# Performance work log

Measured on AMD Instinct MI355X. Metric: run time of the kernel, lower is better.

Reference implementation:

```python
import jax, jax.numpy as jnp
import numpy as np

LN_EPS = 1e-5


def setup_inputs() -> dict:
    key = jax.random.key(0)
    ks = jax.random.split(key, 6)
    N, E, D = 100000, 600000, 128
    x = jax.random.normal(ks[0], (N, D), dtype=jnp.float32)
    edge_index = jax.random.randint(ks[1], (2, E), 0, N, dtype=jnp.int64)
    dropout_mask = jax.random.uniform(ks[2], (N, D), dtype=jnp.float32)
    ln_gamma = jnp.ones((D,), dtype=jnp.float32)
    ln_beta = jnp.zeros((D,), dtype=jnp.float32)
    W_l = jax.random.normal(ks[3], (D, D), dtype=jnp.float32) / np.sqrt(D)
    b_l = jnp.zeros((D,), dtype=jnp.float32)
    W_r = jax.random.normal(ks[4], (D, D), dtype=jnp.float32) / np.sqrt(D)
    return {"x": x, "edge_index": edge_index, "dropout_mask": dropout_mask,
            "ln_gamma": ln_gamma, "ln_beta": ln_beta,
            "W_l": W_l, "b_l": b_l, "W_r": W_r}


def reference(x, edge_index, dropout_mask, ln_gamma, ln_beta, W_l, b_l, W_r):
    N = x.shape[0]
    # LayerNorm (elementwise affine) -> ReLU -> dropout mask
    mu = jnp.mean(x, axis=-1, keepdims=True)
    var = jnp.mean(jnp.square(x - mu), axis=-1, keepdims=True)
    h = (x - mu) * jax.lax.rsqrt(var + LN_EPS) * ln_gamma + ln_beta
    h = jax.nn.relu(h) * dropout_mask  # [N, D]
    # SAGEConv with mean aggregation: messages flow src -> dst
    src, dst = edge_index[0], edge_index[1]
    agg = jax.ops.segment_sum(h[src], dst, num_segments=N)  # [N, D]
    cnt = jax.ops.segment_sum(jnp.ones_like(dst, dtype=h.dtype), dst,
                              num_segments=N)
    mean_agg = agg / jnp.maximum(cnt, 1.0)[:, None]
    # out = lin_l(mean_agg) + lin_r(h); PyG stores weights as [out, in]
    return mean_agg @ W_l.T + b_l + h @ W_r.T
```

## Files before the change

### kernel.cpp

```cpp
#include <hip/hip_runtime.h>

#define LN_EPS 1e-5f
#define D 128
#define SCAN_CHUNK 1024
#define LDSA_STRIDE 264

typedef __attribute__((ext_vector_type(4))) float f32x4;
typedef __attribute__((ext_vector_type(8))) short bf16x8;

static __device__ __forceinline__ ushort f2bf(float f) {
    union { float f; unsigned u; } a; a.f = f;
    unsigned r = a.u + 0x7FFF + ((a.u >> 16) & 1);
    return (ushort)(r >> 16);
}
static __device__ __forceinline__ float bf2f(ushort u) {
    union { unsigned u; float f; } a; a.u = ((unsigned)u) << 16;
    return a.f;
}

__global__ void prep_w(const float* __restrict__ Wl,
                       const float* __restrict__ Wr,
                       ushort* __restrict__ Bfrag,
                       int* __restrict__ hist,
                       int* __restrict__ csums, int N) {
    int t = blockIdx.x * blockDim.x + threadIdx.x;
    if (t < 8 * 8 * 64 * 8) {
        int i    = t & 7;
        int lane = (t >> 3) & 63;
        int jb   = (t >> 9) & 7;
        int ks   = t >> 12;
        int k = ks * 32 + (lane >> 4) * 8 + i;
        int j = jb * 16 + (lane & 15);
        float v = (k < D) ? Wl[j * D + k] : Wr[j * D + (k - D)];
        Bfrag[t] = f2bf(v);
    }
    if (t < 128) csums[t] = 0;
    for (int i = t; i < N; i += gridDim.x * blockDim.x) hist[i] = 0;
}

__global__ void hist_k(const int* __restrict__ ei, int* __restrict__ hist, int E) {
    int base = (blockIdx.x * blockDim.x + threadIdx.x) * 4;
    const int* dst = ei + E;
    if (base + 3 < E) {
        int4 d = *(const int4*)(dst + base);
        atomicAdd(&hist[d.x], 1);
        atomicAdd(&hist[d.y], 1);
        atomicAdd(&hist[d.z], 1);
        atomicAdd(&hist[d.w], 1);
    } else {
        for (int i = base; i < E && i < base + 4; i++)
            atomicAdd(&hist[dst[i]], 1);
    }
}

__global__ void scan_all(const int* __restrict__ hist, int* __restrict__ offs,
                         int* __restrict__ cursor, int* __restrict__ csums, int N) {
    __shared__ int lds[256];
    __shared__ int base_s;
    int base = blockIdx.x * SCAN_CHUNK;
    int t = threadIdx.x;
    int idx0 = base + t * 4;
    int v[4];
#pragma unroll
    for (int i = 0; i < 4; i++) {
        int idx = idx0 + i;
        v[i] = (idx < N) ? hist[idx] : 0;
    }
    lds[t] = v[0] + v[1] + v[2] + v[3];
    __syncthreads();
    for (int off = 1; off < 256; off <<= 1) {
        int add = (t >= off) ? lds[t - off] : 0;
        __syncthreads();
        lds[t] += add;
        __syncthreads();
    }
    int run = (t == 0) ? 0 : lds[t - 1];
    if (t == 255)
        __hip_atomic_store(&csums[blockIdx.x], lds[255] | 0x40000000,
                           __ATOMIC_RELEASE, __HIP_MEMORY_SCOPE_AGENT);
    if (t < 64) {
        int acc = 0;
        for (int c = t; c < (int)blockIdx.x; c += 64) {
            int w;
            do {
                w = __hip_atomic_load(&csums[c], __ATOMIC_ACQUIRE,
                                      __HIP_MEMORY_SCOPE_AGENT);
            } while (!(w & 0x40000000));
            acc += w & 0x3FFFFFFF;
        }
#pragma unroll
        for (int off = 32; off > 0; off >>= 1) acc += __shfl_xor(acc, off);
        if (t == 0) base_s = acc;
    }
    __syncthreads();
    run += base_s;
#pragma unroll
    for (int i = 0; i < 4; i++) {
        int idx = idx0 + i;
        if (idx < N) {
            offs[idx] = run;
            cursor[idx] = run;
        }
        run += v[i];
    }
}

__global__ void sort_edges(const int* __restrict__ ei, int* __restrict__ cursor,
                           int* __restrict__ sorted_src, int E) {
    int base = (blockIdx.x * blockDim.x + threadIdx.x) * 4;
    if (base >= E) return;
    if (base + 3 < E) {
        int4 d = *(const int4*)(ei + E + base);
        int4 s = *(const int4*)(ei + base);
        int p0 = atomicAdd(&cursor[d.x], 1);
        int p1 = atomicAdd(&cursor[d.y], 1);
        int p2 = atomicAdd(&cursor[d.z], 1);
        int p3 = atomicAdd(&cursor[d.w], 1);
        sorted_src[p0] = s.x;
        sorted_src[p1] = s.y;
        sorted_src[p2] = s.z;
        sorted_src[p3] = s.w;
    } else {
        for (int e = base; e < E; e++) {
            int pos = atomicAdd(&cursor[ei[E + e]], 1);
            sorted_src[pos] = ei[e];
        }
    }
}

__global__ void ln_k(const float* __restrict__ x,
                     const float* __restrict__ mask,
                     const float* __restrict__ gamma,
                     const float* __restrict__ beta,
                     ushort* __restrict__ hbf, int N) {
    int tid  = threadIdx.x;
    int lane = tid & 63;
    int wid  = ((int)blockIdx.x * 256 + tid) >> 6;
    int g2   = lane >> 4;
    int sl   = lane & 15;
    int node = wid * 4 + g2;
    if (node >= N) return;

    const float* xr = x + (size_t)node * D + sl * 8;
    f32x4 v0 = *(const f32x4*)xr;
    f32x4 v1 = *(const f32x4*)(xr + 4);
    const float* mr = mask + (size_t)node * D + sl * 8;
    f32x4 m0 = *(const f32x4*)mr;
    f32x4 m1 = *(const f32x4*)(mr + 4);

    float s  = (v0.x + v0.y) + (v0.z + v0.w) + (v1.x + v1.y) + (v1.z + v1.w);
    float ss = (v0.x * v0.x + v0.y * v0.y) + (v0.z * v0.z + v0.w * v0.w)
             + (v1.x * v1.x + v1.y * v1.y) + (v1.z * v1.z + v1.w * v1.w);
#pragma unroll
    for (int off = 8; off > 0; off >>= 1) {
        s  += __shfl_xor(s, off);
        ss += __shfl_xor(ss, off);
    }
    float mu  = s * (1.0f / D);
    float var = ss * (1.0f / D) - mu * mu;
    float rs  = rsqrtf(var + LN_EPS);

    f32x4 g0 = *(const f32x4*)(gamma + sl * 8);
    f32x4 g1 = *(const f32x4*)(gamma + sl * 8 + 4);
    f32x4 b0 = *(const f32x4*)(beta + sl * 8);
    f32x4 b1 = *(const f32x4*)(beta + sl * 8 + 4);

    bf16x8 o;
    o[0] = (short)f2bf(fmaxf((v0.x - mu) * rs * g0.x + b0.x, 0.0f) * m0.x);
    o[1] = (short)f2bf(fmaxf((v0.y - mu) * rs * g0.y + b0.y, 0.0f) * m0.y);
    o[2] = (short)f2bf(fmaxf((v0.z - mu) * rs * g0.z + b0.z, 0.0f) * m0.z);
    o[3] = (short)f2bf(fmaxf((v0.w - mu) * rs * g0.w + b0.w, 0.0f) * m0.w);
    o[4] = (short)f2bf(fmaxf((v1.x - mu) * rs * g1.x + b1.x, 0.0f) * m1.x);
    o[5] = (short)f2bf(fmaxf((v1.y - mu) * rs * g1.y + b1.y, 0.0f) * m1.y);
    o[6] = (short)f2bf(fmaxf((v1.z - mu) * rs * g1.z + b1.z, 0.0f) * m1.z);
    o[7] = (short)f2bf(fmaxf((v1.w - mu) * rs * g1.w + b1.w, 0.0f) * m1.w);
    *(bf16x8*)(hbf + (size_t)node * D + sl * 8) = o;
}

__global__ void __launch_bounds__(256, 4)
agg_gemm(float* __restrict__ out,
         const ushort* __restrict__ hbf,
         const int* __restrict__ sorted_src,
         const int* __restrict__ offs,
         const int* __restrict__ hist,
         const ushort* __restrict__ Bfrag,
         const float* __restrict__ bl,
         int N, int E) {
    __shared__ ushort Alds[64 * LDSA_STRIDE];
    int tid  = threadIdx.x;
    int wave = tid >> 6;
    int lane = tid & 63;
    int n0 = blockIdx.x * 64;

#pragma unroll
    for (int it = 0; it < 4; it++) {
        int chunk = tid + 256 * it;
        int row = chunk >> 4;
        int c8  = chunk & 15;
        int node = n0 + row;
        bf16x8 vh = (bf16x8){0,0,0,0,0,0,0,0};
        if (node < N) vh = *(const bf16x8*)(hbf + (size_t)node * D + c8 * 8);
        *(bf16x8*)&Alds[row * LDSA_STRIDE + 128 + c8 * 8] = vh;
    }

    int g  = lane >> 4;
    int sl = lane & 15;
    int row0 = wave * 16 + g;
    int start[4], deg[4], dm1[4];
#pragma unroll
    for (int p = 0; p < 4; p++) {
        int node = n0 + row0 + p * 4;
        start[p] = 0; deg[p] = 0;
        if (node < N) { start[p] = offs[node]; deg[p] = hist[node]; }
        dm1[p] = deg[p] - 1; if (dm1[p] < 0) dm1[p] = 0;
    }
    float acc[4][8];
#pragma unroll
    for (int p = 0; p < 4; p++)
#pragma unroll
        for (int q = 0; q < 8; q++) acc[p][q] = 0.0f;

    int dmax = max(max(deg[0], deg[1]), max(deg[2], deg[3]));
    int Em = E - 1;
    int ia[4], ib[4];
#pragma unroll
    for (int p = 0; p < 4; p++) {
        int pa = start[p];                         if (pa > Em) pa = Em;
        int j1 = (1 < dm1[p]) ? 1 : dm1[p];
        int pb = start[p] + j1;                    if (pb > Em) pb = Em;
        ia[p] = sorted_src[pa];
        ib[p] = sorted_src[pb];
    }
    for (int j = 0; j < dmax; j += 2) {
        int ca[4], cb[4];
#pragma unroll
        for (int p = 0; p < 4; p++) { ca[p] = ia[p]; cb[p] = ib[p]; }
#pragma unroll
        for (int p = 0; p < 4; p++) {
            int j2 = (j + 2 < dm1[p]) ? j + 2 : dm1[p];
            int j3 = (j + 3 < dm1[p]) ? j + 3 : dm1[p];
            int pa = start[p] + j2; if (pa > Em) pa = Em;
            int pb = start[p] + j3; if (pb > Em) pb = Em;
            ia[p] = sorted_src[pa];
            ib[p] = sorted_src[pb];
        }
#pragma unroll
        for (int p = 0; p < 4; p++) {
            bf16x8 v = *(const bf16x8*)(hbf + (size_t)ca[p] * D + sl * 8);
            float m = (j < deg[p]) ? 1.0f : 0.0f;
#pragma unroll
            for (int q = 0; q < 8; q++) acc[p][q] += bf2f((ushort)v[q]) * m;
        }
#pragma unroll
        for (int p = 0; p < 4; p++) {
            bf16x8 v = *(const bf16x8*)(hbf + (size_t)cb[p] * D + sl * 8);
            float m = (j + 1 < deg[p]) ? 1.0f : 0.0f;
#pragma unroll
            for (int q = 0; q < 8; q++) acc[p][q] += bf2f((ushort)v[q]) * m;
        }
    }
#pragma unroll
    for (int p = 0; p < 4; p++) {
        float inv = 1.0f / fmaxf((float)deg[p], 1.0f);
        bf16x8 o;
#pragma unroll
        for (int q = 0; q < 8; q++) o[q] = (short)f2bf(acc[p][q] * inv);
        *(bf16x8*)&Alds[(row0 + p * 4) * LDSA_STRIDE + sl * 8] = o;
    }
    __syncthreads();

    bf16x8 breg[8][2];
#pragma unroll
    for (int ks = 0; ks < 8; ks++)
#pragma unroll
        for (int jj = 0; jj < 2; jj++) {
            int jb = wave * 2 + jj;
            breg[ks][jj] = *(const bf16x8*)(Bfrag + (size_t)((ks * 8 + jb) * 64 + lane) * 8);
        }

    f32x4 acc2[4][2];
#pragma unroll
    for (int nb = 0; nb < 4; nb++)
#pragma unroll
        for (int jj = 0; jj < 2; jj++)
            acc2[nb][jj] = (f32x4){0.f, 0.f, 0.f, 0.f};

    int arow = lane & 15;
    int akoff = (lane >> 4) * 8;
#pragma unroll
    for (int ks = 0; ks < 8; ks++) {
#pragma unroll
        for (int nb = 0; nb < 4; nb++) {
            bf16x8 a = *(const bf16x8*)&Alds[(nb * 16 + arow) * LDSA_STRIDE + ks * 32 + akoff];
            acc2[nb][0] = __builtin_amdgcn_mfma_f32_16x16x32_bf16(a, breg[ks][0], acc2[nb][0], 0, 0, 0);
            acc2[nb][1] = __builtin_amdgcn_mfma_f32_16x16x32_bf16(a, breg[ks][1], acc2[nb][1], 0, 0, 0);
        }
    }

    float bias0 = bl[wave * 32 + (lane & 15)];
    float bias1 = bl[wave * 32 + 16 + (lane & 15)];
    int rbase = (lane >> 4) * 4;
#pragma unroll
    for (int nb = 0; nb < 4; nb++) {
#pragma unroll
        for (int r = 0; r < 4; r++) {
            int row = nb * 16 + rbase + r;
            if (n0 + row < N) {
                float* orow = out + (size_t)(n0 + row) * D + wave * 32 + (lane & 15);
                orow[0]  = acc2[nb][0][r] + bias0;
                orow[16] = acc2[nb][1][r] + bias1;
            }
        }
    }
}

extern "C" void kernel_launch(void* const* d_in, const int* in_sizes, int n_in,
                              void* d_out, int out_size, void* d_ws, size_t ws_size,
                              hipStream_t stream) {
    const float* x     = (const float*)d_in[0];
    const int*   ei    = (const int*)  d_in[1];
    const float* mask  = (const float*)d_in[2];
    const float* gamma = (const float*)d_in[3];
    const float* beta  = (const float*)d_in[4];
    const float* Wl    = (const float*)d_in[5];
    const float* bl    = (const float*)d_in[6];
    const float* Wr    = (const float*)d_in[7];
    float* out = (float*)d_out;

    int N = in_sizes[0] / D;
    int E = in_sizes[1] / 2;
    int chunks = (N + SCAN_CHUNK - 1) / SCAN_CHUNK;

    ushort* hbf   = (ushort*)d_ws;
    ushort* Bfrag = hbf + (size_t)N * D;
    int* hist   = (int*)(Bfrag + 32768);
    int* offs   = hist + N;
    int* cursor = offs + N;
    int* csums  = cursor + N;
    int* ssrc   = csums + 128;

    prep_w<<<512, 256, 0, stream>>>(Wl, Wr, Bfrag, hist, csums, N);
    hist_k<<<(E / 4 + 255) / 256, 256, 0, stream>>>(ei, hist, E);
    scan_all<<<chunks, 256, 0, stream>>>(hist, offs, cursor, csums, N);
    sort_edges<<<(E / 4 + 255) / 256, 256, 0, stream>>>(ei, cursor, ssrc, E);
    ln_k<<<(N + 15) / 16, 256, 0, stream>>>(x, mask, gamma, beta, hbf, N);
    agg_gemm<<<(N + 63) / 64, 256, 0, stream>>>(out, hbf, ssrc, offs, hist, Bfrag,
                                                bl, N, E);
}
```

Before: 261.3 us.

## Fuse prep, histogram, scan, sort and layernorm into one persistent kernel

Merges the weight-prep, histogram, scan, edge-sort and layernorm kernels into a single launch. A small set of persistent blocks runs histogram, scan and sort separated by software grid barriers, while the extra blocks do the weight conversion and layernorm concurrently. Zeroing moves to a memset. This removes several kernel launches and lets the independent layernorm overlap the atomic-bound CSR build. The cost is reliance on spin-wait grid barriers, which need all nph blocks to be co-resident, and only ~98 blocks doing the atomic histogram and sort work.

```diff
diff --git a/kernel.cpp b/kernel.cpp
--- a/kernel.cpp
+++ b/kernel.cpp
@@ -4,6 +4,7 @@
 #define D 128
 #define SCAN_CHUNK 1024
 #define LDSA_STRIDE 264
+#define NBF 128
 
 typedef __attribute__((ext_vector_type(4))) float f32x4;
 typedef __attribute__((ext_vector_type(8))) short bf16x8;
@@ -18,13 +19,80 @@
     return a.f;
 }
 
-__global__ void prep_w(const float* __restrict__ Wl,
-                       const float* __restrict__ Wr,
-                       ushort* __restrict__ Bfrag,
-                       int* __restrict__ hist,
-                       int* __restrict__ csums, int N) {
-    int t = blockIdx.x * blockDim.x + threadIdx.x;
-    if (t < 8 * 8 * 64 * 8) {
+static __device__ __forceinline__ void gbar(int* ctr, int target) {
+    __syncthreads();
+    if (threadIdx.x == 0) {
+        __hip_atomic_fetch_add(ctr, 1, __ATOMIC_ACQ_REL, __HIP_MEMORY_SCOPE_AGENT);
+        while (__hip_atomic_load(ctr, __ATOMIC_ACQUIRE,
+                                 __HIP_MEMORY_SCOPE_AGENT) < target)
+            __builtin_amdgcn_s_sleep(8);
+    }
+    __syncthreads();
+}
+
+__global__ void mega(const float* __restrict__ x, const int* __restrict__ ei,
+                     const float* __restrict__ mask,
+                     const float* __restrict__ gamma,
+                     const float* __restrict__ beta,
+                     const float* __restrict__ Wl,
+                     const float* __restrict__ Wr,
+                     ushort* __restrict__ hbf, ushort* __restrict__ Bfrag,
+                     int* __restrict__ hist, int* __restrict__ offs,
+                     int* __restrict__ cursor, int* __restrict__ csums,
+                     int* __restrict__ bar, int* __restrict__ ssrc,
+                     int N, int E, int nph) {
+    __shared__ int slds[256];
+    __shared__ int base_s;
+    const int bid = (int)blockIdx.x;
+    const int tid = (int)threadIdx.x;
+
+    if (bid >= nph + NBF) {
+        int lane = tid & 63;
+        int wid  = (bid - nph - NBF) * 4 + (tid >> 6);
+        int g2   = lane >> 4;
+        int sl   = lane & 15;
+        int node = wid * 4 + g2;
+        if (node >= N) return;
+
+        const float* xr = x + (size_t)node * D + sl * 8;
+        f32x4 v0 = *(const f32x4*)xr;
+        f32x4 v1 = *(const f32x4*)(xr + 4);
+        const float* mr = mask + (size_t)node * D + sl * 8;
+        f32x4 m0 = *(const f32x4*)mr;
+        f32x4 m1 = *(const f32x4*)(mr + 4);
+
+        float s  = (v0.x + v0.y) + (v0.z + v0.w) + (v1.x + v1.y) + (v1.z + v1.w);
+        float ss = (v0.x * v0.x + v0.y * v0.y) + (v0.z * v0.z + v0.w * v0.w)
+                 + (v1.x * v1.x + v1.y * v1.y) + (v1.z * v1.z + v1.w * v1.w);
+#pragma unroll
+        for (int off = 8; off > 0; off >>= 1) {
+            s  += __shfl_xor(s, off);
+            ss += __shfl_xor(ss, off);
+        }
+        float mu  = s * (1.0f / D);
+        float var = ss * (1.0f / D) - mu * mu;
+        float rs  = rsqrtf(var + LN_EPS);
+
+        f32x4 g0 = *(const f32x4*)(gamma + sl * 8);
+        f32x4 g1 = *(const f32x4*)(gamma + sl * 8 + 4);
+        f32x4 b0 = *(const f32x4*)(beta + sl * 8);
+        f32x4 b1 = *(const f32x4*)(beta + sl * 8 + 4);
+
+        bf16x8 o;
+        o[0] = (short)f2bf(fmaxf((v0.x - mu) * rs * g0.x + b0.x, 0.0f) * m0.x);
+        o[1] = (short)f2bf(fmaxf((v0.y - mu) * rs * g0.y + b0.y, 0.0f) * m0.y);
+        o[2] = (short)f2bf(fmaxf((v0.z - mu) * rs * g0.z + b0.z, 0.0f) * m0.z);
+        o[3] = (short)f2bf(fmaxf((v0.w - mu) * rs * g0.w + b0.w, 0.0f) * m0.w);
+        o[4] = (short)f2bf(fmaxf((v1.x - mu) * rs * g1.x + b1.x, 0.0f) * m1.x);
+        o[5] = (short)f2bf(fmaxf((v1.y - mu) * rs * g1.y + b1.y, 0.0f) * m1.y);
+        o[6] = (short)f2bf(fmaxf((v1.z - mu) * rs * g1.z + b1.z, 0.0f) * m1.z);
+        o[7] = (short)f2bf(fmaxf((v1.w - mu) * rs * g1.w + b1.w, 0.0f) * m1.w);
+        *(bf16x8*)(hbf + (size_t)node * D + sl * 8) = o;
+        return;
+    }
+
+    if (bid >= nph) {
+        int t = (bid - nph) * 256 + tid;
         int i    = t & 7;
         int lane = (t >> 3) & 63;
         int jb   = (t >> 9) & 7;
@@ -33,148 +101,92 @@
         int j = jb * 16 + (lane & 15);
         float v = (k < D) ? Wl[j * D + k] : Wr[j * D + (k - D)];
         Bfrag[t] = f2bf(v);
-    }
-    if (t < 128) csums[t] = 0;
-    for (int i = t; i < N; i += gridDim.x * blockDim.x) hist[i] = 0;
-}
-
-__global__ void hist_k(const int* __restrict__ ei, int* __restrict__ hist, int E) {
-    int base = (blockIdx.x * blockDim.x + threadIdx.x) * 4;
+        return;
+    }
+
+    const int pt  = bid * 256 + tid;
+    const int PTN = nph * 256;
     const int* dst = ei + E;
-    if (base + 3 < E) {
-        int4 d = *(const int4*)(dst + base);
+    const int nq = E >> 2;
+
+    for (int c = pt; c < nq; c += PTN) {
+        int4 d = *(const int4*)(dst + c * 4);
         atomicAdd(&hist[d.x], 1);
         atomicAdd(&hist[d.y], 1);
         atomicAdd(&hist[d.z], 1);
         atomicAdd(&hist[d.w], 1);
-    } else {
-        for (int i = base; i < E && i < base + 4; i++)
-            atomicAdd(&hist[dst[i]], 1);
-    }
-}
-
-__global__ void scan_all(const int* __restrict__ hist, int* __restrict__ offs,
-                         int* __restrict__ cursor, int* __restrict__ csums, int N) {
-    __shared__ int lds[256];
-    __shared__ int base_s;
-    int base = blockIdx.x * SCAN_CHUNK;
-    int t = threadIdx.x;
-    int idx0 = base + t * 4;
-    int v[4];
-#pragma unroll
-    for (int i = 0; i < 4; i++) {
-        int idx = idx0 + i;
-        v[i] = (idx < N) ? hist[idx] : 0;
-    }
-    lds[t] = v[0] + v[1] + v[2] + v[3];
-    __syncthreads();
-    for (int off = 1; off < 256; off <<= 1) {
-        int add = (t >= off) ? lds[t - off] : 0;
+    }
+    for (int e = (nq << 2) + pt; e < E; e += PTN) atomicAdd(&hist[dst[e]], 1);
+    gbar(&bar[0], nph);
+
+    {
+        int base = bid * SCAN_CHUNK;
+        int idx0 = base + tid * 4;
+        int v[4];
+#pragma unroll
+        for (int i = 0; i < 4; i++) {
+            int idx = idx0 + i;
+            v[i] = (idx < N) ? __hip_atomic_load(&hist[idx], __ATOMIC_RELAXED,
+                                                 __HIP_MEMORY_SCOPE_AGENT) : 0;
+        }
+        slds[tid] = v[0] + v[1] + v[2] + v[3];
         __syncthreads();
-        lds[t] += add;
+        for (int off = 1; off < 256; off <<= 1) {
+            int add = (tid >= off) ? slds[tid - off] : 0;
+            __syncthreads();
+            slds[tid] += add;
+            __syncthreads();
+        }
+        int run = (tid == 0) ? 0 : slds[tid - 1];
+        if (tid == 255)
+            __hip_atomic_store(&csums[bid], slds[255] | 0x40000000,
+                               __ATOMIC_RELEASE, __HIP_MEMORY_SCOPE_AGENT);
+        if (tid < 64) {
+            int acc = 0;
+            for (int c = tid; c < bid; c += 64) {
+                int w;
+                do {
+                    w = __hip_atomic_load(&csums[c], __ATOMIC_ACQUIRE,
+                                          __HIP_MEMORY_SCOPE_AGENT);
+                } while (!(w & 0x40000000));
+                acc += w & 0x3FFFFFFF;
+            }
+#pragma unroll
+            for (int off = 32; off > 0; off >>= 1) acc += __shfl_xor(acc, off);
+            if (tid == 0) base_s = acc;
+        }
         __syncthreads();
-    }
-    int run = (t == 0) ? 0 : lds[t - 1];
-    if (t == 255)
-        __hip_atomic_store(&csums[blockIdx.x], lds[255] | 0x40000000,
-                           __ATOMIC_RELEASE, __HIP_MEMORY_SCOPE_AGENT);
-    if (t < 64) {
-        int acc = 0;
-        for (int c = t; c < (int)blockIdx.x; c += 64) {
-            int w;
-            do {
-                w = __hip_atomic_load(&csums[c], __ATOMIC_ACQUIRE,
-                                      __HIP_MEMORY_SCOPE_AGENT);
-            } while (!(w & 0x40000000));
-            acc += w & 0x3FFFFFFF;
-        }
-#pragma unroll
-        for (int off = 32; off > 0; off >>= 1) acc += __shfl_xor(acc, off);
-        if (t == 0) base_s = acc;
-    }
-    __syncthreads();
-    run += base_s;
-#pragma unroll
-    for (int i = 0; i < 4; i++) {
-        int idx = idx0 + i;
-        if (idx < N) {
-            offs[idx] = run;
-            cursor[idx] = run;
-        }
-        run += v[i];
-    }
-}
-
-__global__ void sort_edges(const int* __restrict__ ei, int* __restrict__ cursor,
-                           int* __restrict__ sorted_src, int E) {
-    int base = (blockIdx.x * blockDim.x + threadIdx.x) * 4;
-    if (base >= E) return;
-    if (base + 3 < E) {
-        int4 d = *(const int4*)(ei + E + base);
-        int4 s = *(const int4*)(ei + base);
+        run += base_s;
+#pragma unroll
+        for (int i = 0; i < 4; i++) {
+            int idx = idx0 + i;
+            if (idx < N) {
+                __hip_atomic_store(&offs[idx], run, __ATOMIC_RELAXED,
+                                   __HIP_MEMORY_SCOPE_AGENT);
+                __hip_atomic_store(&cursor[idx], run, __ATOMIC_RELAXED,
+                                   __HIP_MEMORY_SCOPE_AGENT);
+            }
+            run += v[i];
+        }
+    }
+    gbar(&bar[1], nph);
+
+    for (int c = pt; c < nq; c += PTN) {
+        int4 d = *(const int4*)(dst + c * 4);
+        int4 s = *(const int4*)(ei + c * 4);
         int p0 = atomicAdd(&cursor[d.x], 1);
         int p1 = atomicAdd(&cursor[d.y], 1);
         int p2 = atomicAdd(&cursor[d.z], 1);
         int p3 = atomicAdd(&cursor[d.w], 1);
-        sorted_src[p0] = s.x;
-        sorted_src[p1] = s.y;
-        sorted_src[p2] = s.z;
-        sorted_src[p3] = s.w;
-    } else {
-        for (int e = base; e < E; e++) {
-            int pos = atomicAdd(&cursor[ei[E + e]], 1);
-            sorted_src[pos] = ei[e];
-        }
-    }
-}
-
-__global__ void ln_k(const float* __restrict__ x,
-                     const float* __restrict__ mask,
-                     const float* __restrict__ gamma,
-                     const float* __restrict__ beta,
-                     ushort* __restrict__ hbf, int N) {
-    int tid  = threadIdx.x;
-    int lane = tid & 63;
-    int wid  = ((int)blockIdx.x * 256 + tid) >> 6;
-    int g2   = lane >> 4;
-    int sl   = lane & 15;
-    int node = wid * 4 + g2;
-    if (node >= N) return;
-
-    const float* xr = x + (size_t)node * D + sl * 8;
-    f32x4 v0 = *(const f32x4*)xr;
-    f32x4 v1 = *(const f32x4*)(xr + 4);
-    const float* mr = mask + (size_t)node * D + sl * 8;
-    f32x4 m0 = *(const f32x4*)mr;
-    f32x4 m1 = *(const f32x4*)(mr + 4);
-
-    float s  = (v0.x + v0.y) + (v0.z + v0.w) + (v1.x + v1.y) + (v1.z + v1.w);
-    float ss = (v0.x * v0.x + v0.y * v0.y) + (v0.z * v0.z + v0.w * v0.w)
-             + (v1.x * v1.x + v1.y * v1.y) + (v1.z * v1.z + v1.w * v1.w);
-#pragma unroll
-    for (int off = 8; off > 0; off >>= 1) {
-        s  += __shfl_xor(s, off);
-        ss += __shfl_xor(ss, off);
-    }
-    float mu  = s * (1.0f / D);
-    float var = ss * (1.0f / D) - mu * mu;
-    float rs  = rsqrtf(var + LN_EPS);
-
-    f32x4 g0 = *(const f32x4*)(gamma + sl * 8);
-    f32x4 g1 = *(const f32x4*)(gamma + sl * 8 + 4);
-    f32x4 b0 = *(const f32x4*)(beta + sl * 8);
-    f32x4 b1 = *(const f32x4*)(beta + sl * 8 + 4);
-
-    bf16x8 o;
-    o[0] = (short)f2bf(fmaxf((v0.x - mu) * rs * g0.x + b0.x, 0.0f) * m0.x);
-    o[1] = (short)f2bf(fmaxf((v0.y - mu) * rs * g0.y + b0.y, 0.0f) * m0.y);
-    o[2] = (short)f2bf(fmaxf((v0.z - mu) * rs * g0.z + b0.z, 0.0f) * m0.z);
-    o[3] = (short)f2bf(fmaxf((v0.w - mu) * rs * g0.w + b0.w, 0.0f) * m0.w);
-    o[4] = (short)f2bf(fmaxf((v1.x - mu) * rs * g1.x + b1.x, 0.0f) * m1.x);
-    o[5] = (short)f2bf(fmaxf((v1.y - mu) * rs * g1.y + b1.y, 0.0f) * m1.y);
-    o[6] = (short)f2bf(fmaxf((v1.z - mu) * rs * g1.z + b1.z, 0.0f) * m1.z);
-    o[7] = (short)f2bf(fmaxf((v1.w - mu) * rs * g1.w + b1.w, 0.0f) * m1.w);
-    *(bf16x8*)(hbf + (size_t)node * D + sl * 8) = o;
+        ssrc[p0] = s.x;
+        ssrc[p1] = s.y;
+        ssrc[p2] = s.z;
+        ssrc[p3] = s.w;
+    }
+    for (int e = (nq << 2) + pt; e < E; e += PTN) {
+        int pos = atomicAdd(&cursor[dst[e]], 1);
+        ssrc[pos] = ei[e];
+    }
 }
 
 __global__ void __launch_bounds__(256, 4)
@@ -329,21 +341,24 @@
 
     int N = in_sizes[0] / D;
     int E = in_sizes[1] / 2;
-    int chunks = (N + SCAN_CHUNK - 1) / SCAN_CHUNK;
+    int nph = (N + SCAN_CHUNK - 1) / SCAN_CHUNK;
 
     ushort* hbf   = (ushort*)d_ws;
     ushort* Bfrag = hbf + (size_t)N * D;
     int* hist   = (int*)(Bfrag + 32768);
-    int* offs   = hist + N;
+    int* csums  = hist + N;
+    int* bar    = csums + 128;
+    int* offs   = bar + 16;
     int* cursor = offs + N;
-    int* csums  = cursor + N;
-    int* ssrc   = csums + 128;
-
-    prep_w<<<512, 256, 0, stream>>>(Wl, Wr, Bfrag, hist, csums, N);
-    hist_k<<<(E / 4 + 255) / 256, 256, 0, stream>>>(ei, hist, E);
-    scan_all<<<chunks, 256, 0, stream>>>(hist, offs, cursor, csums, N);
-    sort_edges<<<(E / 4 + 255) / 256, 256, 0, stream>>>(ei, cursor, ssrc, E);
-    ln_k<<<(N + 15) / 16, 256, 0, stream>>>(x, mask, gamma, beta, hbf, N);
-    agg_gemm<<<(N + 63) / 64, 256, 0, stream>>>(out, hbf, ssrc, offs, hist, Bfrag,
-                                                bl, N, E);
-}
+    int* ssrc   = cursor + N;
+
+    int lnBlocks = (N + 15) / 16;
+
+    hipMemsetAsync(hist, 0, (size_t)(N + 144) * sizeof(int), stream);
+    mega<<<nph + NBF + lnBlocks, 256, 0, stream>>>(x, ei, mask, gamma, beta,
+                                                   Wl, Wr, hbf, Bfrag, hist,
+                                                   offs, cursor, csums, bar,
+                                                   ssrc, N, E, nph);
+    agg_gemm<<<(N + 63) / 64, 256, 0, stream>>>(out, hbf, ssrc, offs, hist,
+                                                Bfrag, bl, N, E);
+}
```

Result: no change. 257.9 us (-1.3%).

## Fuse LayerNorm, weight packing and histogram into one launch; stage output stores via LDS

Applied to the files above, without the earlier changes.

Merges the LayerNorm, weight-fragment packing and destination histogram kernels into a single launch whose block ranges select the role. Each LN wave now processes two node groups to raise memory-level parallelism, and the zeroing of hist/csums moves to a hipMemsetAsync over a reordered contiguous workspace layout. The GEMM epilogue writes results to LDS first, then emits coalesced 16-byte row stores instead of scattered 4-byte stores. The aim is fewer launches and better store coalescing, at the cost of an extra LDS round trip and two barriers in the epilogue.

```diff
diff --git a/kernel.cpp b/kernel.cpp
--- a/kernel.cpp
+++ b/kernel.cpp
@@ -18,13 +18,37 @@
     return a.f;
 }
 
-__global__ void prep_w(const float* __restrict__ Wl,
-                       const float* __restrict__ Wr,
-                       ushort* __restrict__ Bfrag,
-                       int* __restrict__ hist,
-                       int* __restrict__ csums, int N) {
-    int t = blockIdx.x * blockDim.x + threadIdx.x;
-    if (t < 8 * 8 * 64 * 8) {
+__global__ void ln_pack_hist(const float* __restrict__ x,
+                             const float* __restrict__ mask,
+                             const float* __restrict__ gamma,
+                             const float* __restrict__ beta,
+                             ushort* __restrict__ hbf,
+                             const float* __restrict__ Wl,
+                             const float* __restrict__ Wr,
+                             ushort* __restrict__ Bfrag,
+                             const int* __restrict__ ei,
+                             int* __restrict__ hist,
+                             int N, int E, int lnBlocks, int packBlocks) {
+    int bid = (int)blockIdx.x;
+    int tid = (int)threadIdx.x;
+
+    if (bid >= lnBlocks + packBlocks) {
+        int base = ((bid - lnBlocks - packBlocks) * 256 + tid) * 4;
+        const int* dst = ei + E;
+        if (base + 3 < E) {
+            int4 d = *(const int4*)(dst + base);
+            atomicAdd(&hist[d.x], 1);
+            atomicAdd(&hist[d.y], 1);
+            atomicAdd(&hist[d.z], 1);
+            atomicAdd(&hist[d.w], 1);
+        } else {
+            for (int i = base; i < E && i < base + 4; i++)
+                atomicAdd(&hist[dst[i]], 1);
+        }
+        return;
+    }
+    if (bid >= lnBlocks) {
+        int t = (bid - lnBlocks) * 256 + tid;
         int i    = t & 7;
         int lane = (t >> 3) & 63;
         int jb   = (t >> 9) & 7;
@@ -33,23 +57,78 @@
         int j = jb * 16 + (lane & 15);
         float v = (k < D) ? Wl[j * D + k] : Wr[j * D + (k - D)];
         Bfrag[t] = f2bf(v);
-    }
-    if (t < 128) csums[t] = 0;
-    for (int i = t; i < N; i += gridDim.x * blockDim.x) hist[i] = 0;
-}
-
-__global__ void hist_k(const int* __restrict__ ei, int* __restrict__ hist, int E) {
-    int base = (blockIdx.x * blockDim.x + threadIdx.x) * 4;
-    const int* dst = ei + E;
-    if (base + 3 < E) {
-        int4 d = *(const int4*)(dst + base);
-        atomicAdd(&hist[d.x], 1);
-        atomicAdd(&hist[d.y], 1);
-        atomicAdd(&hist[d.z], 1);
-        atomicAdd(&hist[d.w], 1);
-    } else {
-        for (int i = base; i < E && i < base + 4; i++)
-            atomicAdd(&hist[dst[i]], 1);
+        return;
+    }
+
+    int lane = tid & 63;
+    int wid  = bid * 4 + (tid >> 6);
+    int g2   = lane >> 4;
+    int sl   = lane & 15;
+    int nodeA = wid * 8 + g2;
+    int nodeB = nodeA + 4;
+    if (nodeA >= N) return;
+    int nB = (nodeB < N) ? nodeB : nodeA;
+
+    const float* xa = x + (size_t)nodeA * D + sl * 8;
+    const float* xb = x + (size_t)nB * D + sl * 8;
+    const float* ma = mask + (size_t)nodeA * D + sl * 8;
+    const float* mb = mask + (size_t)nB * D + sl * 8;
+    f32x4 va0 = *(const f32x4*)xa;
+    f32x4 va1 = *(const f32x4*)(xa + 4);
+    f32x4 vb0 = *(const f32x4*)xb;
+    f32x4 vb1 = *(const f32x4*)(xb + 4);
+    f32x4 ma0 = *(const f32x4*)ma;
+    f32x4 ma1 = *(const f32x4*)(ma + 4);
+    f32x4 mb0 = *(const f32x4*)mb;
+    f32x4 mb1 = *(const f32x4*)(mb + 4);
+
+    float sA  = (va0.x + va0.y) + (va0.z + va0.w) + (va1.x + va1.y) + (va1.z + va1.w);
+    float ssA = (va0.x * va0.x + va0.y * va0.y) + (va0.z * va0.z + va0.w * va0.w)
+              + (va1.x * va1.x + va1.y * va1.y) + (va1.z * va1.z + va1.w * va1.w);
+    float sB  = (vb0.x + vb0.y) + (vb0.z + vb0.w) + (vb1.x + vb1.y) + (vb1.z + vb1.w);
+    float ssB = (vb0.x * vb0.x + vb0.y * vb0.y) + (vb0.z * vb0.z + vb0.w * vb0.w)
+              + (vb1.x * vb1.x + vb1.y * vb1.y) + (vb1.z * vb1.z + vb1.w * vb1.w);
+#pragma unroll
+    for (int off = 8; off > 0; off >>= 1) {
+        sA  += __shfl_xor(sA, off);
+        ssA += __shfl_xor(ssA, off);
+        sB  += __shfl_xor(sB, off);
+        ssB += __shfl_xor(ssB, off);
+    }
+    float muA = sA * (1.0f / D);
+    float vrA = ssA * (1.0f / D) - muA * muA;
+    float rsA = rsqrtf(vrA + LN_EPS);
+    float muB = sB * (1.0f / D);
+    float vrB = ssB * (1.0f / D) - muB * muB;
+    float rsB = rsqrtf(vrB + LN_EPS);
+
+    f32x4 g0 = *(const f32x4*)(gamma + sl * 8);
+    f32x4 g1 = *(const f32x4*)(gamma + sl * 8 + 4);
+    f32x4 b0 = *(const f32x4*)(beta + sl * 8);
+    f32x4 b1 = *(const f32x4*)(beta + sl * 8 + 4);
+
+    bf16x8 oA;
+    oA[0] = (short)f2bf(fmaxf((va0.x - muA) * rsA * g0.x + b0.x, 0.0f) * ma0.x);
+    oA[1] = (short)f2bf(fmaxf((va0.y - muA) * rsA * g0.y + b0.y, 0.0f) * ma0.y);
+    oA[2] = (short)f2bf(fmaxf((va0.z - muA) * rsA * g0.z + b0.z, 0.0f) * ma0.z);
+    oA[3] = (short)f2bf(fmaxf((va0.w - muA) * rsA * g0.w + b0.w, 0.0f) * ma0.w);
+    oA[4] = (short)f2bf(fmaxf((va1.x - muA) * rsA * g1.x + b1.x, 0.0f) * ma1.x);
+    oA[5] = (short)f2bf(fmaxf((va1.y - muA) * rsA * g1.y + b1.y, 0.0f) * ma1.y);
+    oA[6] = (short)f2bf(fmaxf((va1.z - muA) * rsA * g1.z + b1.z, 0.0f) * ma1.z);
+    oA[7] = (short)f2bf(fmaxf((va1.w - muA) * rsA * g1.w + b1.w, 0.0f) * ma1.w);
+    *(bf16x8*)(hbf + (size_t)nodeA * D + sl * 8) = oA;
+
+    if (nodeB < N) {
+        bf16x8 oB;
+        oB[0] = (short)f2bf(fmaxf((vb0.x - muB) * rsB * g0.x + b0.x, 0.0f) * mb0.x);
+        oB[1] = (short)f2bf(fmaxf((vb0.y - muB) * rsB * g0.y + b0.y, 0.0f) * mb0.y);
+        oB[2] = (short)f2bf(fmaxf((vb0.z - muB) * rsB * g0.z + b0.z, 0.0f) * mb0.z);
+        oB[3] = (short)f2bf(fmaxf((vb0.w - muB) * rsB * g0.w + b0.w, 0.0f) * mb0.w);
+        oB[4] = (short)f2bf(fmaxf((vb1.x - muB) * rsB * g1.x + b1.x, 0.0f) * mb1.x);
+        oB[5] = (short)f2bf(fmaxf((vb1.y - muB) * rsB * g1.y + b1.y, 0.0f) * mb1.y);
+        oB[6] = (short)f2bf(fmaxf((vb1.z - muB) * rsB * g1.z + b1.z, 0.0f) * mb1.z);
+        oB[7] = (short)f2bf(fmaxf((vb1.w - muB) * rsB * g1.w + b1.w, 0.0f) * mb1.w);
+        *(bf16x8*)(hbf + (size_t)nodeB * D + sl * 8) = oB;
     }
 }
 
@@ -128,55 +207,6 @@
     }
 }
 
-__global__ void ln_k(const float* __restrict__ x,
-                     const float* __restrict__ mask,
-                     const float* __restrict__ gamma,
-                     const float* __restrict__ beta,
-                     ushort* __restrict__ hbf, int N) {
-    int tid  = threadIdx.x;
-    int lane = tid & 63;
-    int wid  = ((int)blockIdx.x * 256 + tid) >> 6;
-    int g2   = lane >> 4;
-    int sl   = lane & 15;
-    int node = wid * 4 + g2;
-    if (node >= N) return;
-
-    const float* xr = x + (size_t)node * D + sl * 8;
-    f32x4 v0 = *(const f32x4*)xr;
-    f32x4 v1 = *(const f32x4*)(xr + 4);
-    const float* mr = mask + (size_t)node * D + sl * 8;
-    f32x4 m0 = *(const f32x4*)mr;
-    f32x4 m1 = *(const f32x4*)(mr + 4);
-
-    float s  = (v0.x + v0.y) + (v0.z + v0.w) + (v1.x + v1.y) + (v1.z + v1.w);
-    float ss = (v0.x * v0.x + v0.y * v0.y) + (v0.z * v0.z + v0.w * v0.w)
-             + (v1.x * v1.x + v1.y * v1.y) + (v1.z * v1.z + v1.w * v1.w);
-#pragma unroll
-    for (int off = 8; off > 0; off >>= 1) {
-        s  += __shfl_xor(s, off);
-        ss += __shfl_xor(ss, off);
-    }
-    float mu  = s * (1.0f / D);
-    float var = ss * (1.0f / D) - mu * mu;
-    float rs  = rsqrtf(var + LN_EPS);
-
-    f32x4 g0 = *(const f32x4*)(gamma + sl * 8);
-    f32x4 g1 = *(const f32x4*)(gamma + sl * 8 + 4);
-    f32x4 b0 = *(const f32x4*)(beta + sl * 8);
-    f32x4 b1 = *(const f32x4*)(beta + sl * 8 + 4);
-
-    bf16x8 o;
-    o[0] = (short)f2bf(fmaxf((v0.x - mu) * rs * g0.x + b0.x, 0.0f) * m0.x);
-    o[1] = (short)f2bf(fmaxf((v0.y - mu) * rs * g0.y + b0.y, 0.0f) * m0.y);
-    o[2] = (short)f2bf(fmaxf((v0.z - mu) * rs * g0.z + b0.z, 0.0f) * m0.z);
-    o[3] = (short)f2bf(fmaxf((v0.w - mu) * rs * g0.w + b0.w, 0.0f) * m0.w);
-    o[4] = (short)f2bf(fmaxf((v1.x - mu) * rs * g1.x + b1.x, 0.0f) * m1.x);
-    o[5] = (short)f2bf(fmaxf((v1.y - mu) * rs * g1.y + b1.y, 0.0f) * m1.y);
-    o[6] = (short)f2bf(fmaxf((v1.z - mu) * rs * g1.z + b1.z, 0.0f) * m1.z);
-    o[7] = (short)f2bf(fmaxf((v1.w - mu) * rs * g1.w + b1.w, 0.0f) * m1.w);
-    *(bf16x8*)(hbf + (size_t)node * D + sl * 8) = o;
-}
-
 __global__ void __launch_bounds__(256, 4)
 agg_gemm(float* __restrict__ out,
          const ushort* __restrict__ hbf,
@@ -297,20 +327,30 @@
         }
     }
 
+    __syncthreads();
+    float* fl = (float*)Alds;
     float bias0 = bl[wave * 32 + (lane & 15)];
     float bias1 = bl[wave * 32 + 16 + (lane & 15)];
     int rbase = (lane >> 4) * 4;
+    int c0 = wave * 32 + (lane & 15);
 #pragma unroll
     for (int nb = 0; nb < 4; nb++) {
 #pragma unroll
         for (int r = 0; r < 4; r++) {
             int row = nb * 16 + rbase + r;
-            if (n0 + row < N) {
-                float* orow = out + (size_t)(n0 + row) * D + wave * 32 + (lane & 15);
-                orow[0]  = acc2[nb][0][r] + bias0;
-                orow[16] = acc2[nb][1][r] + bias1;
-            }
-        }
+            fl[row * 128 + c0]      = acc2[nb][0][r] + bias0;
+            fl[row * 128 + c0 + 16] = acc2[nb][1][r] + bias1;
+        }
+    }
+    __syncthreads();
+#pragma unroll
+    for (int it = 0; it < 8; it++) {
+        int c = tid + it * 256;
+        int row = c >> 5;
+        int q   = c & 31;
+        if (n0 + row < N)
+            *(f32x4*)(out + (size_t)(n0 + row) * D + q * 4) =
+                *(const f32x4*)&fl[row * 128 + q * 4];
     }
 }
 
@@ -334,16 +374,21 @@
     ushort* hbf   = (ushort*)d_ws;
     ushort* Bfrag = hbf + (size_t)N * D;
     int* hist   = (int*)(Bfrag + 32768);
-    int* offs   = hist + N;
+    int* csums  = hist + N;
+    int* offs   = csums + 128;
     int* cursor = offs + N;
-    int* csums  = cursor + N;
-    int* ssrc   = csums + 128;
-
-    prep_w<<<512, 256, 0, stream>>>(Wl, Wr, Bfrag, hist, csums, N);
-    hist_k<<<(E / 4 + 255) / 256, 256, 0, stream>>>(ei, hist, E);
+    int* ssrc   = cursor + N;
+
+    int lnBlocks   = (N + 31) / 32;
+    int packBlocks = 128;
+    int histBlocks = (E + 1023) / 1024;
+
+    hipMemsetAsync(hist, 0, (size_t)(N + 128) * sizeof(int), stream);
+    ln_pack_hist<<<lnBlocks + packBlocks + histBlocks, 256, 0, stream>>>(
+        x, mask, gamma, beta, hbf, Wl, Wr, Bfrag, ei, hist, N, E,
+        lnBlocks, packBlocks);
     scan_all<<<chunks, 256, 0, stream>>>(hist, offs, cursor, csums, N);
     sort_edges<<<(E / 4 + 255) / 256, 256, 0, stream>>>(ei, cursor, ssrc, E);
-    ln_k<<<(N + 15) / 16, 256, 0, stream>>>(x, mask, gamma, beta, hbf, N);
-    agg_gemm<<<(N + 63) / 64, 256, 0, stream>>>(out, hbf, ssrc, offs, hist, Bfrag,
-                                                bl, N, E);
-}
+    agg_gemm<<<(N + 63) / 64, 256, 0, stream>>>(out, hbf, ssrc, offs, hist,
+                                                Bfrag, bl, N, E);
+}
```

After: 255.0 us. -2.4%, faster.
